# Kernel tuning notes

Measured on AMD Instinct MI355X. Metric: run time of the kernel, lower is better.

## Reference

```python
import jax, jax.numpy as jnp
import numpy as np

DROPOUT_P = 0.5  # pre-softmax dropout prob from __init__
_MASK_KEY = jax.random.key(42)  # fixed key -> deterministic dropout mask


def setup_inputs() -> dict:
    key = jax.random.key(0)
    kq, kk, kv = jax.random.split(key, 3)
    shape = (4, 16, 1024, 64)  # [B, H, S, D]
    Q = jax.random.normal(kq, shape, dtype=jnp.float32)
    K = jax.random.normal(kk, shape, dtype=jnp.float32)
    V = jax.random.normal(kv, shape, dtype=jnp.float32)
    return {"Q": Q, "K": K, "V": V}


def reference(Q, K, V):
    # scores: [B, H, S, S] = Q @ K^T  (no 1/sqrt(d) scaling: scale=False)
    scores = jnp.einsum("bhqd,bhkd->bhqk", Q, K)
    # pre-softmax dropout (train mode, p=0.5), deterministic fixed-key mask
    keep = jax.random.bernoulli(_MASK_KEY, 1.0 - DROPOUT_P, scores.shape)
    scores = jnp.where(keep, scores / (1.0 - DROPOUT_P), 0.0)
    attn = jax.nn.softmax(scores, axis=-1)
    return jnp.einsum("bhqk,bhkd->bhqd", attn, V)
```

## Files before the change

kernel.cpp:

```cpp
#include <hip/hip_runtime.h>
#include <hip/hip_bf16.h>
#include <hip/hip_fp16.h>
#include <math.h>

typedef _Float16 f16x8 __attribute__((ext_vector_type(8)));
typedef __fp16  h16x2 __attribute__((ext_vector_type(2)));
typedef float f32x4 __attribute__((ext_vector_type(4)));

#define S_LEN 1024
#define DH 64
#define KVB 64
#define NIT 16
#define PROW 68
#define THR 11.0f

__device__ __forceinline__ unsigned rotl(unsigned x, unsigned r) {
  return __builtin_amdgcn_alignbit(x, x, 32u - r);
}

__device__ __forceinline__ bool keep_bit(unsigned e) {
  const unsigned ks1 = 42u;
  const unsigned ks2 = 0x1BD11BF0u;
  unsigned x0 = 0u;
  unsigned x1 = e + ks1;
#define TFR(Ra,Rb,Rc,Rd) \
  x0 += x1; x1 = rotl(x1, Ra); x1 ^= x0; \
  x0 += x1; x1 = rotl(x1, Rb); x1 ^= x0; \
  x0 += x1; x1 = rotl(x1, Rc); x1 ^= x0; \
  x0 += x1; x1 = rotl(x1, Rd); x1 ^= x0;
  TFR(13u,15u,26u, 6u)  x0 += ks1; x1 += ks2 + 1u;
  TFR(17u,29u,16u,24u)  x0 += ks2; x1 += 2u;
  TFR(13u,15u,26u, 6u)     x1 += ks1 + 3u;
  TFR(17u,29u,16u,24u)  x0 += ks1; x1 += ks2 + 4u;
  TFR(13u,15u,26u, 6u)  x0 += ks2; x1 += 5u;
#undef TFR
  return ((x0 ^ x1) >> 31) == 0u;
}

__device__ __forceinline__ f16x8 pk8(f32x4 a, f32x4 b) {
  h16x2 p0 = __builtin_amdgcn_cvt_pkrtz(a[0], a[1]);
  h16x2 p1 = __builtin_amdgcn_cvt_pkrtz(a[2], a[3]);
  h16x2 p2 = __builtin_amdgcn_cvt_pkrtz(b[0], b[1]);
  h16x2 p3 = __builtin_amdgcn_cvt_pkrtz(b[2], b[3]);
  f16x8 r;
  r[0]=(_Float16)p0[0]; r[1]=(_Float16)p0[1]; r[2]=(_Float16)p1[0]; r[3]=(_Float16)p1[1];
  r[4]=(_Float16)p2[0]; r[5]=(_Float16)p2[1]; r[6]=(_Float16)p3[0]; r[7]=(_Float16)p3[1];
  return r;
}

__global__ __launch_bounds__(256)
void attn_dropout_kernel(const float* __restrict__ Q, const float* __restrict__ K,
                         const float* __restrict__ V, float* __restrict__ out) {
  __shared__ _Float16 Pl[4][16][PROW];

  const unsigned bh   = blockIdx.x >> 4;
  const unsigned q0   = (blockIdx.x & 15u) * 64u;
  const unsigned tid  = threadIdx.x;
  const unsigned w    = tid >> 6;
  const unsigned lane = tid & 63u;
  const unsigned g    = lane >> 4;
  const unsigned ln   = lane & 15u;
  const unsigned qw   = q0 + w * 16u;

  f16x8 Qa0, Qa1;
  {
    const float* Qp = Q + (size_t)(bh * S_LEN + qw + ln) * DH + g * 8;
    const float s = 2.885390082f;
    f32x4 a = *(const f32x4*)(Qp)      * s;
    f32x4 b = *(const f32x4*)(Qp + 4)  * s;
    f32x4 c = *(const f32x4*)(Qp + 32) * s;
    f32x4 d = *(const f32x4*)(Qp + 36) * s;
    Qa0 = pk8(a, b);
    Qa1 = pk8(c, d);
  }

  float mrun[4], lpart[4];
  f32x4 accO[4];
#pragma unroll
  for (int r = 0; r < 4; ++r) { mrun[r] = -1e30f; lpart[r] = 0.0f; }
#pragma unroll
  for (int n = 0; n < 4; ++n) accO[n] = (f32x4){0.f, 0.f, 0.f, 0.f};

  const float* Kb = K + ((size_t)bh * S_LEN + ln) * DH + g * 8;
  const float* Vb = V + ((size_t)bh * S_LEN + g * 8) * DH + ln;

  for (int t = 0; t < NIT; ++t) {
    f32x4 sc[4];
    {
      const float* Kt = Kb + (size_t)t * KVB * DH;
#pragma unroll
      for (int nt = 0; nt < 4; ++nt) {
        const float* Kp = Kt + nt * 16 * DH;
        f32x4 a = *(const f32x4*)(Kp);
        f32x4 b = *(const f32x4*)(Kp + 4);
        f32x4 c = *(const f32x4*)(Kp + 32);
        f32x4 d = *(const f32x4*)(Kp + 36);
        f16x8 kb0 = pk8(a, b);
        f16x8 kb1 = pk8(c, d);
        f32x4 acc = (f32x4){0.f, 0.f, 0.f, 0.f};
        acc = __builtin_amdgcn_mfma_f32_16x16x32_f16(Qa0, kb0, acc, 0, 0, 0);
        acc = __builtin_amdgcn_mfma_f32_16x16x32_f16(Qa1, kb1, acc, 0, 0, 0);
        sc[nt] = acc;
      }
    }

    float sm[4][4];
    float pmx[4];
#pragma unroll
    for (int r = 0; r < 4; ++r) pmx[r] = -1e30f;
#pragma unroll
    for (int nt = 0; nt < 4; ++nt) {
#pragma unroll
      for (int r = 0; r < 4; ++r) {
        unsigned q  = qw + g * 4 + r;
        unsigned kg = (unsigned)t * KVB + nt * 16 + ln;
        unsigned e  = (bh << 20) + (q << 10) + kg;
        float v = keep_bit(e) ? sc[nt][r] : 0.0f;
        sm[nt][r] = v;
        pmx[r] = fmaxf(pmx[r], v);
      }
    }

    bool need = (pmx[0] > mrun[0] + THR) | (pmx[1] > mrun[1] + THR) |
                (pmx[2] > mrun[2] + THR) | (pmx[3] > mrun[3] + THR);
    if (__any(need)) {
#pragma unroll
      for (int r = 0; r < 4; ++r) {
        float mx = pmx[r];
#pragma unroll
        for (int off = 1; off < 16; off <<= 1) mx = fmaxf(mx, __shfl_xor(mx, off));
        float mn  = fmaxf(mrun[r], mx);
        float scl = exp2f(mrun[r] - mn);
        mrun[r] = mn;
        lpart[r] *= scl;
#pragma unroll
        for (int n = 0; n < 4; ++n) accO[n][r] *= scl;
      }
    }

    f32x4 va[4], vbx[4], vc[4], vd[4];
    {
      const float* Vt = Vb + (size_t)t * KVB * DH;
#pragma unroll
      for (int nd = 0; nd < 4; ++nd) {
#pragma unroll
        for (int j = 0; j < 4; ++j) {
          va[nd][j]  = Vt[(j)      * DH + nd * 16];
          vbx[nd][j] = Vt[(4 + j)  * DH + nd * 16];
          vc[nd][j]  = Vt[(32 + j) * DH + nd * 16];
          vd[nd][j]  = Vt[(36 + j) * DH + nd * 16];
        }
      }
    }

#pragma unroll
    for (int nt = 0; nt < 4; ++nt) {
#pragma unroll
      for (int r = 0; r < 4; ++r) {
        float p = exp2f(sm[nt][r] - mrun[r]);
        lpart[r] += p;
        Pl[w][g * 4 + r][nt * 16 + ln] = (_Float16)p;
      }
    }

    f16x8 Pa0 = *(const f16x8*)&Pl[w][ln][g * 8];
    f16x8 Pa1 = *(const f16x8*)&Pl[w][ln][32 + g * 8];
#pragma unroll
    for (int nd = 0; nd < 4; ++nd) {
      f16x8 v0 = pk8(va[nd], vbx[nd]);
      f16x8 v1 = pk8(vc[nd], vd[nd]);
      accO[nd] = __builtin_amdgcn_mfma_f32_16x16x32_f16(Pa0, v0, accO[nd], 0, 0, 0);
      accO[nd] = __builtin_amdgcn_mfma_f32_16x16x32_f16(Pa1, v1, accO[nd], 0, 0, 0);
    }
  }

  float lf[4];
#pragma unroll
  for (int r = 0; r < 4; ++r) {
    float l = lpart[r];
#pragma unroll
    for (int off = 1; off < 16; off <<= 1) l += __shfl_xor(l, off);
    lf[r] = l;
  }
#pragma unroll
  for (int nd = 0; nd < 4; ++nd) {
#pragma unroll
    for (int r = 0; r < 4; ++r) {
      unsigned q = qw + g * 4 + r;
      out[(size_t)(bh * S_LEN + q) * DH + nd * 16 + ln] = accO[nd][r] / lf[r];
    }
  }
}

extern "C" void kernel_launch(void* const* d_in, const int* in_sizes, int n_in,
                              void* d_out, int out_size, void* d_ws, size_t ws_size,
                              hipStream_t stream) {
  const float* Q = (const float*)d_in[0];
  const float* K = (const float*)d_in[1];
  const float* V = (const float*)d_in[2];
  float* out = (float*)d_out;
  dim3 grid(64 * 16);
  dim3 block(256);
  hipLaunchKernelGGL(attn_dropout_kernel, grid, block, 0, stream, Q, K, V, out);
}
```

Baseline: 256.5 us.

## Split KV tile across two wave groups per block and merge softmax states

Doubles the block to 512 threads: each query strip of 16 rows is now handled by two waves, each covering half of every 64-key tile. At the end the two partial online-softmax states (max, sum, output accumulator) are merged through shared memory. This halves per-wave work per iteration, which shortens the serial loop and adds latency hiding. The cost is an extra shared-memory merge, two barriers, more registers pressure per block and fewer blocks resident per CU.

```diff
diff --git a/kernel.cpp b/kernel.cpp
--- a/kernel.cpp
+++ b/kernel.cpp
@@ -11,7 +11,7 @@
 #define DH 64
 #define KVB 64
 #define NIT 16
-#define PROW 68
+#define PROW 36
 #define THR 11.0f
 
 __device__ __forceinline__ unsigned rotl(unsigned x, unsigned r) {
@@ -48,10 +48,13 @@
   return r;
 }
 
-__global__ __launch_bounds__(256)
+__global__ __launch_bounds__(512)
 void attn_dropout_kernel(const float* __restrict__ Q, const float* __restrict__ K,
                          const float* __restrict__ V, float* __restrict__ out) {
-  __shared__ _Float16 Pl[4][16][PROW];
+  __shared__ __align__(16) char smem[64*68*4 + 64*2*4];
+  _Float16* Pl = (_Float16*)smem;
+  float* Om = (float*)smem;
+  float* Ml = (float*)(smem + 64*68*4);
 
   const unsigned bh   = blockIdx.x >> 4;
   const unsigned q0   = (blockIdx.x & 15u) * 64u;
@@ -60,7 +63,9 @@
   const unsigned lane = tid & 63u;
   const unsigned g    = lane >> 4;
   const unsigned ln   = lane & 15u;
-  const unsigned qw   = q0 + w * 16u;
+  const unsigned p    = w & 3u;
+  const unsigned koff = (w >> 2) * 32u;
+  const unsigned qw   = q0 + p * 16u;
 
   f16x8 Qa0, Qa1;
   {
@@ -81,15 +86,15 @@
 #pragma unroll
   for (int n = 0; n < 4; ++n) accO[n] = (f32x4){0.f, 0.f, 0.f, 0.f};
 
-  const float* Kb = K + ((size_t)bh * S_LEN + ln) * DH + g * 8;
-  const float* Vb = V + ((size_t)bh * S_LEN + g * 8) * DH + ln;
+  const float* Kb = K + ((size_t)bh * S_LEN + koff + ln) * DH + g * 8;
+  const float* Vb = V + ((size_t)bh * S_LEN + koff + g * 8) * DH + ln;
 
   for (int t = 0; t < NIT; ++t) {
-    f32x4 sc[4];
+    f32x4 sc[2];
     {
       const float* Kt = Kb + (size_t)t * KVB * DH;
 #pragma unroll
-      for (int nt = 0; nt < 4; ++nt) {
+      for (int nt = 0; nt < 2; ++nt) {
         const float* Kp = Kt + nt * 16 * DH;
         f32x4 a = *(const f32x4*)(Kp);
         f32x4 b = *(const f32x4*)(Kp + 4);
@@ -104,22 +109,19 @@
       }
     }
 
-    float sm[4][4];
+#pragma unroll
+    for (int nt = 0; nt < 2; ++nt) {
+#pragma unroll
+      for (int r = 0; r < 4; ++r) {
+        unsigned q  = qw + g * 4 + r;
+        unsigned kg = (unsigned)t * KVB + koff + nt * 16 + ln;
+        unsigned e  = (bh << 20) + (q << 10) + kg;
+        sc[nt][r] = keep_bit(e) ? sc[nt][r] : 0.0f;
+      }
+    }
     float pmx[4];
 #pragma unroll
-    for (int r = 0; r < 4; ++r) pmx[r] = -1e30f;
-#pragma unroll
-    for (int nt = 0; nt < 4; ++nt) {
-#pragma unroll
-      for (int r = 0; r < 4; ++r) {
-        unsigned q  = qw + g * 4 + r;
-        unsigned kg = (unsigned)t * KVB + nt * 16 + ln;
-        unsigned e  = (bh << 20) + (q << 10) + kg;
-        float v = keep_bit(e) ? sc[nt][r] : 0.0f;
-        sm[nt][r] = v;
-        pmx[r] = fmaxf(pmx[r], v);
-      }
-    }
+    for (int r = 0; r < 4; ++r) pmx[r] = fmaxf(sc[0][r], sc[1][r]);
 
     bool need = (pmx[0] > mrun[0] + THR) | (pmx[1] > mrun[1] + THR) |
                 (pmx[2] > mrun[2] + THR) | (pmx[3] > mrun[3] + THR);
@@ -138,57 +140,81 @@
       }
     }
 
-    f32x4 va[4], vbx[4], vc[4], vd[4];
+    f32x4 va[4], vbx[4];
     {
       const float* Vt = Vb + (size_t)t * KVB * DH;
 #pragma unroll
       for (int nd = 0; nd < 4; ++nd) {
 #pragma unroll
         for (int j = 0; j < 4; ++j) {
-          va[nd][j]  = Vt[(j)      * DH + nd * 16];
-          vbx[nd][j] = Vt[(4 + j)  * DH + nd * 16];
-          vc[nd][j]  = Vt[(32 + j) * DH + nd * 16];
-          vd[nd][j]  = Vt[(36 + j) * DH + nd * 16];
+          va[nd][j]  = Vt[(j)     * DH + nd * 16];
+          vbx[nd][j] = Vt[(4 + j) * DH + nd * 16];
         }
       }
     }
 
 #pragma unroll
-    for (int nt = 0; nt < 4; ++nt) {
-#pragma unroll
-      for (int r = 0; r < 4; ++r) {
-        float p = exp2f(sm[nt][r] - mrun[r]);
-        lpart[r] += p;
-        Pl[w][g * 4 + r][nt * 16 + ln] = (_Float16)p;
-      }
-    }
-
-    f16x8 Pa0 = *(const f16x8*)&Pl[w][ln][g * 8];
-    f16x8 Pa1 = *(const f16x8*)&Pl[w][ln][32 + g * 8];
+    for (int nt = 0; nt < 2; ++nt) {
+#pragma unroll
+      for (int r = 0; r < 4; ++r) {
+        float pv = exp2f(sc[nt][r] - mrun[r]);
+        lpart[r] += pv;
+        Pl[(w * 16 + g * 4 + r) * PROW + nt * 16 + ln] = (_Float16)pv;
+      }
+    }
+
+    f16x8 Pa = *(const f16x8*)&Pl[(w * 16 + ln) * PROW + g * 8];
 #pragma unroll
     for (int nd = 0; nd < 4; ++nd) {
       f16x8 v0 = pk8(va[nd], vbx[nd]);
-      f16x8 v1 = pk8(vc[nd], vd[nd]);
-      accO[nd] = __builtin_amdgcn_mfma_f32_16x16x32_f16(Pa0, v0, accO[nd], 0, 0, 0);
-      accO[nd] = __builtin_amdgcn_mfma_f32_16x16x32_f16(Pa1, v1, accO[nd], 0, 0, 0);
-    }
-  }
-
-  float lf[4];
+      accO[nd] = __builtin_amdgcn_mfma_f32_16x16x32_f16(Pa, v0, accO[nd], 0, 0, 0);
+    }
+  }
+
 #pragma unroll
   for (int r = 0; r < 4; ++r) {
     float l = lpart[r];
 #pragma unroll
     for (int off = 1; off < 16; off <<= 1) l += __shfl_xor(l, off);
-    lf[r] = l;
-  }
-#pragma unroll
-  for (int nd = 0; nd < 4; ++nd) {
+    lpart[r] = l;
+  }
+
+  __syncthreads();
+  if (w >= 4) {
+#pragma unroll
+    for (int nd = 0; nd < 4; ++nd)
+#pragma unroll
+      for (int r = 0; r < 4; ++r)
+        Om[(p * 16 + g * 4 + r) * 68 + nd * 16 + ln] = accO[nd][r];
+    if (ln == 0) {
+#pragma unroll
+      for (int r = 0; r < 4; ++r) {
+        Ml[(p * 16 + g * 4 + r) * 2 + 0] = mrun[r];
+        Ml[(p * 16 + g * 4 + r) * 2 + 1] = lpart[r];
+      }
+    }
+  }
+  __syncthreads();
+  if (w < 4) {
+    float e1[4], e2[4], lf[4];
 #pragma unroll
     for (int r = 0; r < 4; ++r) {
-      unsigned q = qw + g * 4 + r;
-      out[(size_t)(bh * S_LEN + q) * DH + nd * 16 + ln] = accO[nd][r] / lf[r];
-    }
+      const unsigned row = p * 16 + g * 4 + r;
+      float m2 = Ml[row * 2 + 0];
+      float l2 = Ml[row * 2 + 1];
+      float m  = fmaxf(mrun[r], m2);
+      e1[r] = exp2f(mrun[r] - m);
+      e2[r] = exp2f(m2 - m);
+      lf[r] = lpart[r] * e1[r] + l2 * e2[r];
+    }
+#pragma unroll
+    for (int nd = 0; nd < 4; ++nd)
+#pragma unroll
+      for (int r = 0; r < 4; ++r) {
+        const unsigned row = p * 16 + g * 4 + r;
+        float o = accO[nd][r] * e1[r] + Om[row * 68 + nd * 16 + ln] * e2[r];
+        out[(size_t)(bh * S_LEN + q0 + row) * DH + nd * 16 + ln] = o / lf[r];
+      }
   }
 }
 
@@ -200,6 +226,6 @@
   const float* V = (const float*)d_in[2];
   float* out = (float*)d_out;
   dim3 grid(64 * 16);
-  dim3 block(256);
+  dim3 block(512);
   hipLaunchKernelGGL(attn_dropout_kernel, grid, block, 0, stream, Q, K, V, out);
 }
```

New measurement: 254.4 us. About the same (-0.8%).
